# Optimization experiments

Measured on AMD Instinct MI355X. Metric: run time of the kernel, lower is better.

Reference implementation:

```python
import jax, jax.numpy as jnp
import numpy as np

OUT_SIZE = 7        # output_size (7, 7)
RATIO = 2           # RoIAlign sampling_ratio
FINEST = 56.0       # finest_scale
SCALES = (0.25, 0.125, 0.0625, 0.03125)  # FPN spatial scales, strides 4/8/16/32
IMG_H, IMG_W = 800, 1216
NUM_ROIS = 1024


def _roi_align(feat, rois, scale):
    """RoIAlign (torchvision legacy, aligned=False) for one level.
    feat: [C, H, W]; rois: [4, K] xyxy in image coords. Returns [K, C, 7, 7]."""
    C, H, W = feat.shape
    K = rois.shape[1]
    x1, y1, x2, y2 = rois * scale
    roi_w = jnp.maximum(x2 - x1, 1.0)
    roi_h = jnp.maximum(y2 - y1, 1.0)
    S = OUT_SIZE * RATIO  # 14 sample points per spatial dim
    g = (jnp.arange(S, dtype=feat.dtype) + 0.5) / RATIO  # offsets in bin units
    ys = y1[:, None] + g[None, :] * (roi_h / OUT_SIZE)[:, None]  # [K, S]
    xs = x1[:, None] + g[None, :] * (roi_w / OUT_SIZE)[:, None]  # [K, S]
    # points outside [-1, H]x[-1, W] contribute 0 (torchvision semantics)
    vy = (ys >= -1.0) & (ys <= H)
    vx = (xs >= -1.0) & (xs <= W)
    valid = vy[:, :, None] & vx[:, None, :]  # [K, S, S]
    y = jnp.clip(ys, 0.0, H - 1)
    x = jnp.clip(xs, 0.0, W - 1)
    y0f = jnp.floor(y)
    x0f = jnp.floor(x)
    y0 = y0f.astype(jnp.int32)
    x0 = x0f.astype(jnp.int32)
    yh = jnp.minimum(y0 + 1, H - 1)
    xh = jnp.minimum(x0 + 1, W - 1)
    wy = (y - y0f)[:, None, :, None]  # [K,1,S,1]
    wx = (x - x0f)[:, None, None, :]  # [K,1,1,S]
    ff = feat.reshape(C, H * W)

    def gather(yi, xi):  # yi,xi: [K,S] -> [K,C,S,S]
        idx = yi[:, :, None] * W + xi[:, None, :]  # [K,S,S]
        return jnp.transpose(ff[:, idx], (1, 0, 2, 3))

    v00 = gather(y0, x0)
    v01 = gather(y0, xh)
    v10 = gather(yh, x0)
    v11 = gather(yh, xh)
    val = (v00 * (1.0 - wy) * (1.0 - wx) + v01 * (1.0 - wy) * wx
           + v10 * wy * (1.0 - wx) + v11 * wy * wx)
    val = val * valid[:, None, :, :].astype(val.dtype)
    # average the RATIO x RATIO samples per output bin
    out = val.reshape(K, C, OUT_SIZE, RATIO, OUT_SIZE, RATIO).mean(axis=(3, 5))
    return out


def _map_levels(rois, n_lvls):
    scale = jnp.sqrt((rois[2] - rois[0] + 1.0) * (rois[3] - rois[1] + 1.0))
    lv = jnp.floor(jnp.log2(scale / FINEST + 1e-6))
    return jnp.clip(lv, 0, n_lvls - 1).astype(jnp.int32)


def setup_inputs() -> dict:
    key = jax.random.key(0)
    ks = jax.random.split(key, 8)
    feat0 = jax.random.normal(ks[0], (256, 200, 304), dtype=jnp.float32)
    feat1 = jax.random.normal(ks[1], (256, 100, 152), dtype=jnp.float32)
    feat2 = jax.random.normal(ks[2], (256, 50, 76), dtype=jnp.float32)
    feat3 = jax.random.normal(ks[3], (256, 25, 38), dtype=jnp.float32)
    cx = jax.random.uniform(ks[4], (NUM_ROIS,), minval=0.0, maxval=float(IMG_W))
    cy = jax.random.uniform(ks[5], (NUM_ROIS,), minval=0.0, maxval=float(IMG_H))
    w = jnp.exp(jax.random.uniform(ks[6], (NUM_ROIS,), minval=np.log(16.0), maxval=np.log(640.0)))
    h = jnp.exp(jax.random.uniform(ks[7], (NUM_ROIS,), minval=np.log(16.0), maxval=np.log(640.0)))
    x1 = jnp.clip(cx - w / 2, 0.0, IMG_W - 1.0)
    x2 = jnp.clip(cx + w / 2, 0.0, IMG_W - 1.0)
    y1 = jnp.clip(cy - h / 2, 0.0, IMG_H - 1.0)
    y2 = jnp.clip(cy + h / 2, 0.0, IMG_H - 1.0)
    rois = jnp.stack([x1, y1, x2, y2]).astype(jnp.float32)  # [4, K]
    return {"feat0": feat0, "feat1": feat1, "feat2": feat2, "feat3": feat3, "rois": rois}


def reference(feat0, feat1, feat2, feat3, rois):
    feats = (feat0, feat1, feat2, feat3)
    n_lvls = len(feats)
    tar = _map_levels(rois, n_lvls)  # [K] target FPN level per RoI
    K = rois.shape[1]
    C = feat0.shape[0]
    out = jnp.zeros((K, C, OUT_SIZE, OUT_SIZE), dtype=feat0.dtype)
    for i in range(n_lvls):  # fixed small loop over structurally distinct levels
        lvl_out = _roi_align(feats[i], rois, SCALES[i])
        out = out + jnp.where((tar == i)[:, None, None, None], lvl_out, 0.0)
    return out
```

## Files before the change

kernel.cpp:

```cpp
#include <hip/hip_runtime.h>
#include <math.h>

#define OUTS 7
#define NBIN 49
#define NCH 256
#define LDSW 1200
#define OBS 132

#define O1 15564800ull
#define O2 19456000ull
#define O3 20428800ull
#define WS_FLOATS 20672000ull
#define WS_BYTES  (WS_FLOATS * 4ull)

__global__ __launch_bounds__(256) void transpose_cl(
    const float* __restrict__ f0, const float* __restrict__ f1,
    const float* __restrict__ f2, const float* __restrict__ f3,
    float* __restrict__ ws)
{
    const int bt = blockIdx.x;
    const int cb = blockIdx.y * 64;
    const float* src; float* dst; int HW, t0;
    if (bt < 950)       { src = f0; dst = ws;      HW = 60800; t0 = bt; }
    else if (bt < 1188) { src = f1; dst = ws + O1; HW = 15200; t0 = bt - 950; }
    else if (bt < 1248) { src = f2; dst = ws + O2; HW = 3800;  t0 = bt - 1188; }
    else                { src = f3; dst = ws + O3; HW = 950;   t0 = bt - 1248; }
    const int hw0 = t0 * 64;

    __shared__ float tile[64][65];
    const int tx = threadIdx.x & 63;
    const int ty = threadIdx.x >> 6;

#pragma unroll
    for (int j = 0; j < 16; ++j) {
        const int c = cb + ty + 4 * j;
        const int hw = hw0 + tx;
        tile[ty + 4 * j][tx] = (hw < HW) ? src[(size_t)c * HW + hw] : 0.0f;
    }
    __syncthreads();
#pragma unroll
    for (int j = 0; j < 16; ++j) {
        const int hw = hw0 + ty + 4 * j;
        if (hw < HW) dst[(size_t)hw * 256 + cb + tx] = tile[tx][ty + 4 * j];
    }
}

__global__ __launch_bounds__(256) void roi_main(
    const float* __restrict__ ws, const float* __restrict__ rois,
    float* __restrict__ out, int K)
{
    const int k = blockIdx.x;
    const int cbase = blockIdx.y * 128;
    const int tid = threadIdx.x;
    const int wid = tid >> 6;
    const int lane = tid & 63;

    const float rx1 = rois[0 * K + k];
    const float ry1 = rois[1 * K + k];
    const float rx2 = rois[2 * K + k];
    const float ry2 = rois[3 * K + k];

    const float sroi = sqrtf((rx2 - rx1 + 1.0f) * (ry2 - ry1 + 1.0f));
    int lv = (int)floorf(log2f(sroi / 56.0f + 1e-6f));
    lv = lv < 0 ? 0 : (lv > 3 ? 3 : lv);

    const float* wb; int H, W; float sc;
    switch (lv) {
        case 0:  wb = ws;      H = 200; W = 304; sc = 0.25f;    break;
        case 1:  wb = ws + O1; H = 100; W = 152; sc = 0.125f;   break;
        case 2:  wb = ws + O2; H = 50;  W = 76;  sc = 0.0625f;  break;
        default: wb = ws + O3; H = 25;  W = 38;  sc = 0.03125f; break;
    }

    const float y1s = ry1 * sc;
    const float ystep = fmaxf(ry2 * sc - y1s, 1.0f) / (float)OUTS;
    const float x1s = rx1 * sc;
    const float xstep = fmaxf(rx2 * sc - x1s, 1.0f) / (float)OUTS;

    __shared__ int2   syo[14];  __shared__ float2 syw[14];
    __shared__ int2   sxo[14];  __shared__ float2 sxw[14];
    __shared__ float  obuf[NBIN * OBS];

    if (tid < 14) {
        const int s = tid;
        const float g = ((float)s + 0.5f) * 0.5f;
        const float ysv = y1s + g * ystep;
        const float v = (ysv >= -1.0f && ysv <= (float)H) ? 0.5f : 0.0f;
        const float y = fminf(fmaxf(ysv, 0.0f), (float)(H - 1));
        const float yf = floorf(y);
        const int y0 = (int)yf;
        const float wy = y - yf;
        syo[s] = make_int2(y0 * W, min(y0 + 1, H - 1) * W);
        syw[s] = make_float2((1.0f - wy) * v, wy * v);
    } else if (tid < 28) {
        const int s = tid - 14;
        const float g = ((float)s + 0.5f) * 0.5f;
        const float xsv = x1s + g * xstep;
        const float v = (xsv >= -1.0f && xsv <= (float)W) ? 0.5f : 0.0f;
        const float x = fminf(fmaxf(xsv, 0.0f), (float)(W - 1));
        const float xf = floorf(x);
        const int x0 = (int)xf;
        const float wx = x - xf;
        sxo[s] = make_int2(x0, min(x0 + 1, W - 1));
        sxw[s] = make_float2((1.0f - wx) * v, wx * v);
    }
    __syncthreads();

    const float* wbl = wb + cbase + 2 * lane;

    for (int b = wid; b < NBIN; b += 4) {
        const int oh = b / OUTS;
        const int ow = b - oh * OUTS;

        const int2   ya = syo[2 * oh], yb = syo[2 * oh + 1];
        const float2 wa = syw[2 * oh], wbv = syw[2 * oh + 1];
        const int2   xa = sxo[2 * ow], xb = sxo[2 * ow + 1];
        const float2 ua = sxw[2 * ow], ub = sxw[2 * ow + 1];

        const int   yo[4] = { ya.x, ya.y, yb.x, yb.y };
        const float yw[4] = { wa.x, wa.y, wbv.x, wbv.y };
        const int   xo[4] = { xa.x, xa.y, xb.x, xb.y };
        const float xw[4] = { ua.x, ua.y, ub.x, ub.y };

        float a0 = 0.0f, a1 = 0.0f;
#pragma unroll
        for (int iy = 0; iy < 4; ++iy) {
#pragma unroll
            for (int ix = 0; ix < 4; ++ix) {
                const float2 v = *(const float2*)(wbl + ((size_t)(yo[iy] + xo[ix]) << 8));
                const float wv = yw[iy] * xw[ix];
                a0 += v.x * wv;
                a1 += v.y * wv;
            }
        }
        *(float2*)(&obuf[b * OBS + 2 * lane]) = make_float2(a0, a1);
    }
    __syncthreads();

    float* dst = out + ((size_t)k * NCH + cbase) * NBIN;
    for (int i = tid; i < 128 * NBIN; i += 256) {
        const int c = i / NBIN;
        const int b = i - c * NBIN;
        dst[i] = obuf[b * OBS + c];
    }
}

__global__ __launch_bounds__(256) void roi_extract_fallback(
    const float* __restrict__ f0, const float* __restrict__ f1,
    const float* __restrict__ f2, const float* __restrict__ f3,
    const float* __restrict__ rois, float* __restrict__ out, int K)
{
    const int k = blockIdx.x;
    if (k >= K) return;
    const int cbase = blockIdx.y * 32;
    const int tid = threadIdx.x;
    const int wid = tid >> 6;
    const int lane = tid & 63;
    const int bin = lane < NBIN ? lane : NBIN - 1;

    const float rx1 = rois[0 * K + k];
    const float ry1 = rois[1 * K + k];
    const float rx2 = rois[2 * K + k];
    const float ry2 = rois[3 * K + k];

    const float sroi = sqrtf((rx2 - rx1 + 1.0f) * (ry2 - ry1 + 1.0f));
    int lv = (int)floorf(log2f(sroi / 56.0f + 1e-6f));
    lv = lv < 0 ? 0 : (lv > 3 ? 3 : lv);

    const float* fbase; int H, W; float sc;
    switch (lv) {
        case 0:  fbase = f0; H = 200; W = 304; sc = 0.25f;    break;
        case 1:  fbase = f1; H = 100; W = 152; sc = 0.125f;   break;
        case 2:  fbase = f2; H = 50;  W = 76;  sc = 0.0625f;  break;
        default: fbase = f3; H = 25;  W = 38;  sc = 0.03125f; break;
    }
    const int HW = H * W;

    const float y1s = ry1 * sc;
    const float roih = fmaxf(ry2 * sc - y1s, 1.0f);
    const float x1s = rx1 * sc;
    const float roiw = fmaxf(rx2 * sc - x1s, 1.0f);
    const float ystep = roih / (float)OUTS;
    const float xstep = roiw / (float)OUTS;

    const float ysA = y1s + 0.25f * ystep, ysZ = y1s + 6.75f * ystep;
    const float xsA = x1s + 0.25f * xstep, xsZ = x1s + 6.75f * xstep;
    const int ylo = (int)floorf(fminf(fmaxf(ysA, 0.0f), (float)(H - 1)));
    const int xlo = (int)floorf(fminf(fmaxf(xsA, 0.0f), (float)(W - 1)));
    const int xhi = min((int)floorf(fminf(fmaxf(xsZ, 0.0f), (float)(W - 1))) + 1, W - 1);
    const int yhi = min((int)floorf(fminf(fmaxf(ysZ, 0.0f), (float)(H - 1))) + 1, H - 1);
    const int Ww = xhi - xlo + 1;
    const int Hw = yhi - ylo + 1;
    const int E = Ww * Hw;
    const bool useLds = (E <= LDSW);
    const int stride = useLds ? Ww : W;
    const int obase  = useLds ? 0 : (ylo * W + xlo);

    const int oh = bin / OUTS;
    const int ow = bin - oh * OUTS;

    int ry0[2], ry1i[2]; float wy[2], vy[2];
#pragma unroll
    for (int py = 0; py < 2; ++py) {
        const float g = ((float)(oh * 2 + py) + 0.5f) * 0.5f;
        const float ys = y1s + g * ystep;
        vy[py] = (ys >= -1.0f && ys <= (float)H) ? 1.0f : 0.0f;
        const float y = fminf(fmaxf(ys, 0.0f), (float)(H - 1));
        const float y0f = floorf(y);
        const int y0 = (int)y0f;
        ry0[py]  = y0 - ylo;
        ry1i[py] = min(y0 + 1, H - 1) - ylo;
        wy[py] = y - y0f;
    }
    int rx0[2], rx1i[2]; float wx[2], vx[2];
#pragma unroll
    for (int px = 0; px < 2; ++px) {
        const float g = ((float)(ow * 2 + px) + 0.5f) * 0.5f;
        const float xs = x1s + g * xstep;
        vx[px] = (xs >= -1.0f && xs <= (float)W) ? 1.0f : 0.0f;
        const float x = fminf(fmaxf(xs, 0.0f), (float)(W - 1));
        const float x0f = floorf(x);
        const int x0 = (int)x0f;
        rx0[px]  = x0 - xlo;
        rx1i[px] = min(x0 + 1, W - 1) - xlo;
        wx[px] = x - x0f;
    }

    int off[16]; float wt[16];
#pragma unroll
    for (int py = 0; py < 2; ++py) {
#pragma unroll
        for (int px = 0; px < 2; ++px) {
            const int i = (py * 2 + px) * 4;
            const float v = vy[py] * vx[px] * 0.25f;
            const float a = wy[py], b = wx[px];
            off[i + 0] = ry0[py]  * stride + rx0[px]  + obase; wt[i + 0] = (1.0f - a) * (1.0f - b) * v;
            off[i + 1] = ry0[py]  * stride + rx1i[px] + obase; wt[i + 1] = (1.0f - a) * b * v;
            off[i + 2] = ry1i[py] * stride + rx0[px]  + obase; wt[i + 2] = a * (1.0f - b) * v;
            off[i + 3] = ry1i[py] * stride + rx1i[px] + obase; wt[i + 3] = a * b * v;
        }
    }

    __shared__ float2 lds2[4 * LDSW];
    float2* const myw = &lds2[wid * LDSW];
    const float inv_Ww = 1.0f / (float)Ww;

#pragma unroll
    for (int j = 0; j < 4; ++j) {
        const int chA = cbase + wid * 8 + j * 2;
        const float* sA = fbase + (size_t)chA * HW + (size_t)ylo * W + xlo;
        const float* sB = sA + HW;

        if (useLds) {
            for (int e = lane; e < E; e += 64) {
                const int r = (int)(((float)e + 0.5f) * inv_Ww);
                const int g = r * W + (e - r * Ww);
                myw[e] = make_float2(sA[g], sB[g]);
            }
            if (lane < NBIN) {
                float ax = 0.0f, ay = 0.0f;
#pragma unroll
                for (int i = 0; i < 16; ++i) {
                    const float2 v = myw[off[i]];
                    ax += v.x * wt[i];
                    ay += v.y * wt[i];
                }
                float* outA = out + ((size_t)k * NCH + chA) * NBIN + bin;
                outA[0] = ax;
                outA[NBIN] = ay;
            }
        } else {
            if (lane < NBIN) {
                const float* pA = fbase + (size_t)chA * HW;
                const float* pB = pA + HW;
                float ax = 0.0f, ay = 0.0f;
#pragma unroll
                for (int i = 0; i < 16; ++i) {
                    ax += pA[off[i]] * wt[i];
                    ay += pB[off[i]] * wt[i];
                }
                float* outA = out + ((size_t)k * NCH + chA) * NBIN + bin;
                outA[0] = ax;
                outA[NBIN] = ay;
            }
        }
    }
}

extern "C" void kernel_launch(void* const* d_in, const int* in_sizes, int n_in,
                              void* d_out, int out_size, void* d_ws, size_t ws_size,
                              hipStream_t stream) {
    const float* f0 = (const float*)d_in[0];
    const float* f1 = (const float*)d_in[1];
    const float* f2 = (const float*)d_in[2];
    const float* f3 = (const float*)d_in[3];
    const float* rois = (const float*)d_in[4];
    float* out = (float*)d_out;
    int K = in_sizes[4] / 4;
    if (K <= 0) return;

    if (ws_size >= WS_BYTES) {
        float* ws = (float*)d_ws;
        transpose_cl<<<dim3(1263, 4), 256, 0, stream>>>(f0, f1, f2, f3, ws);
        roi_main<<<dim3(K, 2), 256, 0, stream>>>(ws, rois, out, K);
    } else {
        roi_extract_fallback<<<dim3(K, 8), 256, 0, stream>>>(f0, f1, f2, f3, rois, out, K);
    }
}
```

Baseline: 189.1 us.

## Store channel-last feature workspace in fp16 and widen RoI blocks to 512 threads

The transposed channel-last workspace now holds fp16 instead of fp32, which halves the bytes written by the transpose and the bytes gathered by the RoI kernel; values are converted back to float for accumulation. The RoI kernel runs 512 threads (8 waves over the 49 bins), and its shared output buffer is laid out channel-major so the final store becomes a contiguous float4 copy. The cost is reduced feature precision (fp16 rounding) against an fp32 reference, plus LDS bank conflicts on the strided obuf writes.

```diff
diff --git a/kernel.cpp b/kernel.cpp
--- a/kernel.cpp
+++ b/kernel.cpp
@@ -1,11 +1,11 @@
 #include <hip/hip_runtime.h>
+#include <hip/hip_fp16.h>
 #include <math.h>
 
 #define OUTS 7
 #define NBIN 49
 #define NCH 256
 #define LDSW 1200
-#define OBS 132
 
 #define O1 15564800ull
 #define O2 19456000ull
@@ -16,11 +16,11 @@
 __global__ __launch_bounds__(256) void transpose_cl(
     const float* __restrict__ f0, const float* __restrict__ f1,
     const float* __restrict__ f2, const float* __restrict__ f3,
-    float* __restrict__ ws)
+    __half* __restrict__ ws)
 {
     const int bt = blockIdx.x;
     const int cb = blockIdx.y * 64;
-    const float* src; float* dst; int HW, t0;
+    const float* src; __half* dst; int HW, t0;
     if (bt < 950)       { src = f0; dst = ws;      HW = 60800; t0 = bt; }
     else if (bt < 1188) { src = f1; dst = ws + O1; HW = 15200; t0 = bt - 950; }
     else if (bt < 1248) { src = f2; dst = ws + O2; HW = 3800;  t0 = bt - 1188; }
@@ -38,15 +38,22 @@
         tile[ty + 4 * j][tx] = (hw < HW) ? src[(size_t)c * HW + hw] : 0.0f;
     }
     __syncthreads();
-#pragma unroll
-    for (int j = 0; j < 16; ++j) {
-        const int hw = hw0 + ty + 4 * j;
-        if (hw < HW) dst[(size_t)hw * 256 + cb + tx] = tile[tx][ty + 4 * j];
+
+    const int cp = threadIdx.x & 31;
+    const int hh = threadIdx.x >> 5;
+#pragma unroll
+    for (int j = 0; j < 8; ++j) {
+        const int hl = hh + 8 * j;
+        const int hw = hw0 + hl;
+        if (hw < HW) {
+            const __half2 h = __floats2half2_rn(tile[2 * cp][hl], tile[2 * cp + 1][hl]);
+            *(__half2*)(dst + (size_t)hw * 256 + cb + 2 * cp) = h;
+        }
     }
 }
 
-__global__ __launch_bounds__(256) void roi_main(
-    const float* __restrict__ ws, const float* __restrict__ rois,
+__global__ __launch_bounds__(512) void roi_main(
+    const __half* __restrict__ ws, const float* __restrict__ rois,
     float* __restrict__ out, int K)
 {
     const int k = blockIdx.x;
@@ -64,7 +71,7 @@
     int lv = (int)floorf(log2f(sroi / 56.0f + 1e-6f));
     lv = lv < 0 ? 0 : (lv > 3 ? 3 : lv);
 
-    const float* wb; int H, W; float sc;
+    const __half* wb; int H, W; float sc;
     switch (lv) {
         case 0:  wb = ws;      H = 200; W = 304; sc = 0.25f;    break;
         case 1:  wb = ws + O1; H = 100; W = 152; sc = 0.125f;   break;
@@ -79,7 +86,7 @@
 
     __shared__ int2   syo[14];  __shared__ float2 syw[14];
     __shared__ int2   sxo[14];  __shared__ float2 sxw[14];
-    __shared__ float  obuf[NBIN * OBS];
+    __shared__ __align__(16) float obuf[128 * NBIN];
 
     if (tid < 14) {
         const int s = tid;
@@ -106,9 +113,9 @@
     }
     __syncthreads();
 
-    const float* wbl = wb + cbase + 2 * lane;
-
-    for (int b = wid; b < NBIN; b += 4) {
+    const __half* wbl = wb + cbase + 2 * lane;
+
+    for (int b = wid; b < NBIN; b += 8) {
         const int oh = b / OUTS;
         const int ow = b - oh * OUTS;
 
@@ -127,22 +134,21 @@
         for (int iy = 0; iy < 4; ++iy) {
 #pragma unroll
             for (int ix = 0; ix < 4; ++ix) {
-                const float2 v = *(const float2*)(wbl + ((size_t)(yo[iy] + xo[ix]) << 8));
+                const __half2 h = *(const __half2*)(wbl + ((size_t)(yo[iy] + xo[ix]) << 8));
+                const float2 v = __half22float2(h);
                 const float wv = yw[iy] * xw[ix];
                 a0 += v.x * wv;
                 a1 += v.y * wv;
             }
         }
-        *(float2*)(&obuf[b * OBS + 2 * lane]) = make_float2(a0, a1);
+        obuf[(2 * lane) * NBIN + b]     = a0;
+        obuf[(2 * lane + 1) * NBIN + b] = a1;
     }
     __syncthreads();
 
-    float* dst = out + ((size_t)k * NCH + cbase) * NBIN;
-    for (int i = tid; i < 128 * NBIN; i += 256) {
-        const int c = i / NBIN;
-        const int b = i - c * NBIN;
-        dst[i] = obuf[b * OBS + c];
-    }
+    const float4* o4 = (const float4*)obuf;
+    float4* d4 = (float4*)(out + ((size_t)k * NCH + cbase) * NBIN);
+    for (int i = tid; i < (128 * NBIN) / 4; i += 512) d4[i] = o4[i];
 }
 
 __global__ __launch_bounds__(256) void roi_extract_fallback(
@@ -300,9 +306,9 @@
     if (K <= 0) return;
 
     if (ws_size >= WS_BYTES) {
-        float* ws = (float*)d_ws;
+        __half* ws = (__half*)d_ws;
         transpose_cl<<<dim3(1263, 4), 256, 0, stream>>>(f0, f1, f2, f3, ws);
-        roi_main<<<dim3(K, 2), 256, 0, stream>>>(ws, rois, out, K);
+        roi_main<<<dim3(K, 2), 512, 0, stream>>>(ws, rois, out, K);
     } else {
         roi_extract_fallback<<<dim3(K, 8), 256, 0, stream>>>(f0, f1, f2, f3, rois, out, K);
     }
```

After: 153.9 us. 1.23x faster.
